# Optimization experiments

Measured on AMD Instinct MI355X. Metric: run time of the kernel, lower is better.

The kernel has to match this reference:

```python
import jax, jax.numpy as jnp
import numpy as np

HEADS = 8
SPLITS = 4


def setup_inputs() -> dict:
    key = jax.random.key(0)
    ks = jax.random.split(key, 5)
    B, C, N = 8, 512, 4096
    C2 = C // 2
    x = jax.random.normal(ks[0], (B, C, N), jnp.float32)
    # reduction: Conv1d(C -> C//2, k=1) => weight [C2, C], bias [C2]
    Wr = jax.random.normal(ks[1], (C2, C), jnp.float32) * (1.0 / np.sqrt(C))
    br = jnp.zeros((C2,), jnp.float32)
    # toQKV: Linear(C2 -> 3*C2, bias=False); stored as [in, out]
    Wqkv = jax.random.normal(ks[2], (C2, 3 * C2), jnp.float32) * (1.0 / np.sqrt(C2))
    # expansion: Conv1d(C2 -> C, k=1) => weight [C, C2], bias [C]
    We = jax.random.normal(ks[3], (C, C2), jnp.float32) * (1.0 / np.sqrt(C2))
    be = jnp.zeros((C,), jnp.float32)
    return {"x": x, "Wr": Wr, "br": br, "Wqkv": Wqkv, "We": We, "be": be}


def reference(x, Wr, br, Wqkv, We, be):
    B, C, N = x.shape
    h, S = HEADS, SPLITS
    # 1x1 conv reduction: [B, C, N] -> [B, C2, N]
    y = jnp.einsum('oc,bcn->bon', Wr, x) + br[None, :, None]
    t = y.transpose(0, 2, 1)                       # [B, N, C2]
    qkv = t @ Wqkv                                 # [B, N, 3*C2]
    q, k, v = jnp.split(qkv, 3, axis=-1)
    d = q.shape[-1] // h
    n = N // S

    def to_chunks(a):
        # b n (h d) -> b h S n' d  (block-diagonal chunks along the token dim)
        return a.reshape(B, N, h, d).transpose(0, 2, 1, 3).reshape(B, h, S, n, d)

    q, k, v = to_chunks(q), to_chunks(k), to_chunks(v)
    scale = d ** -0.5
    scores = jnp.einsum('bhsnd,bhsmd->bhsnm', q, k) * scale   # [B,h,S,n,n]
    attn = jax.nn.softmax(scores, axis=-1)
    o = jnp.einsum('bhsnm,bhsmd->bhsnd', attn, v)             # [B,h,S,n,d]
    # rearrange per-chunk to 'b n (h d)' and concat chunks along n (restores order)
    o = o.transpose(0, 2, 3, 1, 4).reshape(B, N, h * d)       # [B, N, C2]
    o = o.transpose(0, 2, 1)                                  # [B, C2, N]
    out = jnp.einsum('oc,bcn->bon', We, o) + be[None, :, None]  # [B, C, N]
    return out
```

## Files before the change

### kernel.cpp

```cpp
#include <hip/hip_runtime.h>
#include <hip/hip_bf16.h>

#define BATCH 8
#define CIN   512
#define NTOK  4096
#define CH    256
#define J3    768
#define NH    8
#define DH    32
#define NCH   1024

typedef _Float16 F16;
typedef _Float16 f16x8 __attribute__((ext_vector_type(8)));
typedef _Float16 f16x4 __attribute__((ext_vector_type(4)));
typedef _Float16 f16x2 __attribute__((ext_vector_type(2)));
typedef float    f32x4  __attribute__((ext_vector_type(4)));
typedef float    f32x16 __attribute__((ext_vector_type(16)));

#define QSCALE 0.25503483f


__global__ __launch_bounds__(256) void fuse_weights_kernel(
    const float* __restrict__ Wr, const float* __restrict__ br,
    const float* __restrict__ Wqkv,
    F16* __restrict__ Wc_t, float* __restrict__ bcomb)
{
    const int jb8 = blockIdx.x * 8;
    const int c = threadIdx.x;
    float acc0[8], acc1[8];
#pragma unroll
    for (int jj = 0; jj < 8; ++jj) { acc0[jj] = 0.f; acc1[jj] = 0.f; }
    for (int c2 = 0; c2 < CH; ++c2) {
        const float w0 = Wr[c2 * CIN + c];
        const float w1 = Wr[c2 * CIN + c + 256];
#pragma unroll
        for (int jj = 0; jj < 8; ++jj) {
            const float q = Wqkv[c2 * J3 + jb8 + jj];
            acc0[jj] = fmaf(w0, q, acc0[jj]);
            acc1[jj] = fmaf(w1, q, acc1[jj]);
        }
    }
    const int t0 = c >> 5, kg0 = (c >> 3) & 3, e0 = c & 7;
    const int c1 = c + 256;
    const int t1 = c1 >> 5, kg1 = (c1 >> 3) & 3, e1 = c1 & 7;
    const int jb = jb8 >> 8, row0 = jb8 & 255;
#pragma unroll
    for (int jj = 0; jj < 8; ++jj) {
        const float qs = (jb8 + jj < 256) ? QSCALE : 1.0f;
        const int row = row0 + jj;
        Wc_t[jb * 131072 + t0 * 8192 + kg0 * 2048 + row * 8 + e0] =
            (F16)(acc0[jj] * qs);
        Wc_t[jb * 131072 + t1 * 8192 + kg1 * 2048 + row * 8 + e1] =
            (F16)(acc1[jj] * qs);
    }
    if (c < 8) {
        const int j = jb8 + c;
        const float qs = (j < 256) ? QSCALE : 1.0f;
        float s = 0.f;
        for (int c2 = 0; c2 < CH; ++c2) s = fmaf(Wqkv[c2 * J3 + j], br[c2], s);
        bcomb[j] = s * qs;
    }
}

__global__ __launch_bounds__(256) void convert_we_kernel(
    const float* __restrict__ We, F16* __restrict__ We_t)
{
    const int i = blockIdx.x * 256 + threadIdx.x;
    const int j = i >> 8, c2 = i & 255;
    We_t[(j >> 7) * 32768 + (c2 >> 5) * 4096 + ((c2 >> 3) & 3) * 1024 +
         (j & 127) * 8 + (c2 & 7)] = (F16)We[i];
}

__global__ __launch_bounds__(256) void transpose_convert_kernel(
    const float* __restrict__ x, F16* __restrict__ xt_t)
{
    const int b = blockIdx.z;
    const int c0 = blockIdx.y * 8;
    const int n = blockIdx.x * 256 + threadIdx.x;

    const float* xb = x + ((size_t)b * CIN + c0) * NTOK + n;
    f16x8 v;
#pragma unroll
    for (int i = 0; i < 8; ++i)
        v[i] = (F16)xb[(size_t)i * NTOK];

    const int nb = n >> 7, row = n & 127;
    const int t = c0 >> 5, kg = (c0 >> 3) & 3;
    *(f16x8*)&xt_t[(size_t)b * 2097152 + nb * 65536 + t * 4096 + kg * 1024 +
                   row * 8] = v;
}

__global__ __launch_bounds__(512, 4) void gemm1_kernel(
    const F16* __restrict__ A,
    const F16* __restrict__ B,
    const float* __restrict__ bias,
    F16* __restrict__ QKb,
    F16* __restrict__ Vd)
{
    const int b  = blockIdx.z;
    const int jb = blockIdx.y;
    const int j0 = jb * 256;
    const int nb = blockIdx.x;
    const int n0 = nb * 128;
    const int tid = threadIdx.x;
    const int w = tid >> 6, l = tid & 63;
    const int wr = w >> 1;
    const int wc = w & 1;
    const int cl = l & 15, rg = l >> 4;

    __shared__ __align__(16) char smem[49152];
    F16* Ash0 = (F16*)smem;
    F16* Ash1 = (F16*)(smem + 16384);
    F16* Bsh0 = (F16*)(smem + 32768);
    F16* Bsh1 = (F16*)(smem + 40960);
    F16* Esh  = (F16*)smem;

    f32x4 acc[4][4];
#pragma unroll
    for (int i = 0; i < 4; ++i)
#pragma unroll
        for (int j = 0; j < 4; ++j) acc[i][j] = (f32x4){0.f, 0.f, 0.f, 0.f};

    const F16* Abase = A + jb * 131072 + tid * 8;
    const F16* Bbase = B + (size_t)b * 2097152 + nb * 65536 + tid * 8;

#define G1_STAGE(Adst, Bdst, t)                                                \
    do {                                                                       \
        __builtin_amdgcn_global_load_lds(                                      \
            (const __attribute__((address_space(1))) void*)(Abase + (t) * 8192),\
            (__attribute__((address_space(3))) void*)&Adst[tid * 8], 16, 0, 0);\
        __builtin_amdgcn_global_load_lds(                                      \
            (const __attribute__((address_space(1))) void*)(Abase + (t) * 8192 \
                + 4096),                                                       \
            (__attribute__((address_space(3))) void*)&Adst[4096 + tid * 8],    \
            16, 0, 0);                                                         \
        __builtin_amdgcn_global_load_lds(                                      \
            (const __attribute__((address_space(1))) void*)(Bbase + (t) * 4096),\
            (__attribute__((address_space(3))) void*)&Bdst[tid * 8], 16, 0, 0);\
    } while (0)

    G1_STAGE(Ash0, Bsh0, 0);
    __syncthreads();

    for (int t = 0; t < 16; ++t) {
        F16* Ac = (t & 1) ? Ash1 : Ash0;
        F16* Bc = (t & 1) ? Bsh1 : Bsh0;
        if (t < 15) {
            F16* An = (t & 1) ? Ash0 : Ash1;
            F16* Bn = (t & 1) ? Bsh0 : Bsh1;
            G1_STAGE(An, Bn, t + 1);
        }
        f16x8 bf[4];
#pragma unroll
        for (int j = 0; j < 4; ++j)
            bf[j] = *(const f16x8*)&Bc[rg * 1024 + (wc * 64 + j * 16 + cl) * 8];
#pragma unroll
        for (int i = 0; i < 4; ++i) {
            const f16x8 af =
                *(const f16x8*)&Ac[rg * 2048 + (wr * 64 + i * 16 + cl) * 8];
#pragma unroll
            for (int j = 0; j < 4; ++j)
                acc[i][j] = __builtin_amdgcn_mfma_f32_16x16x32_f16(
                    af, bf[j], acc[i][j], 0, 0, 0);
        }
        __syncthreads();
    }
#undef G1_STAGE

    if (j0 < 512) {
        const size_t bN = (size_t)b * NTOK;
#pragma unroll
        for (int c = 0; c < 4; ++c) {
            if (c) __syncthreads();
            if (wc == (c >> 1)) {
#pragma unroll
                for (int i = 0; i < 4; ++i) {
#pragma unroll
                    for (int jj = 0; jj < 2; ++jj) {
                        const int jn = (c & 1) * 2 + jj;
                        const int nl = jj * 16 + cl;
                        const int jl = wr * 64 + i * 16 + rg * 4;
                        const int jg = j0 + jl;
                        f16x4 v;
#pragma unroll
                        for (int r = 0; r < 4; ++r)
                            v[r] = (F16)(acc[i][jn][r] + bias[jg + r]);
                        *(f16x4*)&Esh[nl * 264 + jl] = v;
                    }
                }
            }
            __syncthreads();
            const int rr = tid >> 4, ss = tid & 15;
            const f16x8 ov0 = *(const f16x8*)&Esh[rr * 264 + ss * 16];
            const f16x8 ov1 = *(const f16x8*)&Esh[rr * 264 + ss * 16 + 8];
            F16* dst = &QKb[(bN + n0 + c * 32 + rr) * 512 + j0 + ss * 16];
            *(f16x8*)dst = ov0;
            *(f16x8*)(dst + 8) = ov1;
        }
    } else {
        const size_t bD = (size_t)b * CH;
#pragma unroll
        for (int c = 0; c < 4; ++c) {
            if (c) __syncthreads();
            if (wr == c) {
#pragma unroll
                for (int i = 0; i < 4; ++i) {
                    const int jg = j0 + c * 64 + i * 16 + rg * 4;
#pragma unroll
                    for (int jn = 0; jn < 4; ++jn) {
                        const int nl = wc * 64 + jn * 16 + cl;
#pragma unroll
                        for (int r = 0; r < 4; ++r)
                            Esh[(i * 16 + rg * 4 + r) * 136 + nl] =
                                (F16)(acc[i][jn][r] + bias[jg + r]);
                    }
                }
            }
            __syncthreads();
            const int rr = tid >> 3, ss = tid & 7;
            const f16x8 ov0 = *(const f16x8*)&Esh[rr * 136 + ss * 16];
            const f16x8 ov1 = *(const f16x8*)&Esh[rr * 136 + ss * 16 + 8];
            const int dg = (j0 - 512) + c * 64 + rr;
            F16* dst = &Vd[(bD + dg) * NTOK + n0 + ss * 16];
            *(f16x8*)dst = ov0;
            *(f16x8*)(dst + 8) = ov1;
        }
    }
}

__global__ __launch_bounds__(256) void attn_mfma_kernel(
    const F16* __restrict__ QK,
    const F16* __restrict__ Vd,
    F16* __restrict__ O)
{
    const int bid = blockIdx.x;
    const int xcd = bid & 7, tt = bid >> 3;
    const int qb = tt & 7;
    const int pr = xcd * 32 + (tt >> 3);
    const int s = pr & 3, bh = pr >> 2;
    const int b = bh >> 3, h = bh & 7;
    const int tid = threadIdx.x;
    const int w = tid >> 6, l = tid & 63;
    const int ln = l & 31;
    const int hi = l >> 5;

    __shared__ __align__(16) F16 Klds[2][64 * 40];
    __shared__ __align__(16) F16 Vlds[2][32 * 68];

    const size_t bN = (size_t)b * NTOK + (size_t)s * NCH;
    const int q0 = qb * 128 + w * 32;

    const F16* Qp = QK + (bN + q0 + ln) * 512 + h * DH + hi * 8;
    const f16x8 qf0 = *(const f16x8*)Qp;
    const f16x8 qf1 = *(const f16x8*)(Qp + 16);

    const F16* Kg = QK + (bN + (tid & 63)) * 512 + 256 + h * DH + (tid >> 6) * 8;
    const F16* Vg = Vd + ((size_t)b * CH + h * DH + (tid & 31)) * NTOK
                       + (size_t)s * NCH + (tid >> 5) * 8;
    const int kw = (tid & 63) * 40 + (tid >> 6) * 8;
    const int vw = (tid & 31) * 68 + (tid >> 5) * 8;

    f16x8 kreg = *(const f16x8*)Kg;
    f16x8 vreg = *(const f16x8*)Vg;

    const f16x8 ones = {(F16)1.f, (F16)1.f, (F16)1.f, (F16)1.f,
                        (F16)1.f, (F16)1.f, (F16)1.f, (F16)1.f};

    f32x16 oacc = (f32x16)(0.0f);
    f32x16 lacc = (f32x16)(0.0f);

    *(f16x8*)&Klds[0][kw] = kreg;
    *(f16x4*)&Vlds[0][vw] = __builtin_shufflevector(vreg, vreg, 0, 1, 2, 3);
    *(f16x4*)&Vlds[0][vw + 4] = __builtin_shufflevector(vreg, vreg, 4, 5, 6, 7);

    for (int t = 0; t < 16; ++t) {
        const int cur = t & 1, nxt = cur ^ 1;
        __syncthreads();
        if (t < 15) {
            kreg = *(const f16x8*)(Kg + (size_t)(t + 1) * 64 * 512);
            vreg = *(const f16x8*)(Vg + (t + 1) * 64);
        }
        const F16* Kb = &Klds[cur][0];
        const F16* Vb = &Vlds[cur][0];
#pragma unroll
        for (int u = 0; u < 2; ++u) {
            const int nkb = u * 32;
            const f16x8 kf0 = *(const f16x8*)&Kb[(nkb + ln) * 40 + hi * 8];
            const f16x8 kf1 = *(const f16x8*)&Kb[(nkb + ln) * 40 + 16 + hi * 8];
            f32x16 sacc = (f32x16)(0.0f);
            __builtin_amdgcn_s_setprio(1);
            sacc = __builtin_amdgcn_mfma_f32_32x32x16_f16(kf0, qf0, sacc, 0, 0, 0);
            sacc = __builtin_amdgcn_mfma_f32_32x32x16_f16(kf1, qf1, sacc, 0, 0, 0);
            __builtin_amdgcn_s_setprio(0);

            union { f16x8 v; f16x2 h[4]; } pu0, pu1;
#pragma unroll
            for (int e = 0; e < 4; ++e) {
                pu0.h[e] = __builtin_bit_cast(f16x2, __builtin_amdgcn_cvt_pkrtz(
                    __builtin_amdgcn_exp2f(sacc[2 * e]),
                    __builtin_amdgcn_exp2f(sacc[2 * e + 1])));
                pu1.h[e] = __builtin_bit_cast(f16x2, __builtin_amdgcn_cvt_pkrtz(
                    __builtin_amdgcn_exp2f(sacc[8 + 2 * e]),
                    __builtin_amdgcn_exp2f(sacc[8 + 2 * e + 1])));
            }

            const int vbase = ln * 68 + nkb + 4 * hi;
            const f16x4 v00 = *(const f16x4*)&Vb[vbase];
            const f16x4 v01 = *(const f16x4*)&Vb[vbase + 8];
            const f16x4 v10 = *(const f16x4*)&Vb[vbase + 16];
            const f16x4 v11 = *(const f16x4*)&Vb[vbase + 24];
            const f16x8 vf0 = __builtin_shufflevector(v00, v01, 0, 1, 2, 3, 4, 5, 6, 7);
            const f16x8 vf1 = __builtin_shufflevector(v10, v11, 0, 1, 2, 3, 4, 5, 6, 7);

            __builtin_amdgcn_s_setprio(1);
            oacc = __builtin_amdgcn_mfma_f32_32x32x16_f16(pu0.v, vf0, oacc, 0, 0, 0);
            oacc = __builtin_amdgcn_mfma_f32_32x32x16_f16(pu1.v, vf1, oacc, 0, 0, 0);
            lacc = __builtin_amdgcn_mfma_f32_32x32x16_f16(pu0.v, ones, lacc, 0, 0, 0);
            lacc = __builtin_amdgcn_mfma_f32_32x32x16_f16(pu1.v, ones, lacc, 0, 0, 0);
            __builtin_amdgcn_s_setprio(0);
        }
        if (t < 15) {
            *(f16x8*)&Klds[nxt][kw] = kreg;
            *(f16x4*)&Vlds[nxt][vw] =
                __builtin_shufflevector(vreg, vreg, 0, 1, 2, 3);
            *(f16x4*)&Vlds[nxt][vw + 4] =
                __builtin_shufflevector(vreg, vreg, 4, 5, 6, 7);
        }
    }

    __syncthreads();
    F16* Elds = (F16*)&Klds[0][0] + w * 1152;
#pragma unroll
    for (int r = 0; r < 16; ++r) {
        const int qr = (r & 3) + 8 * (r >> 2) + 4 * hi;
        const float invr = __builtin_amdgcn_rcpf(lacc[r]);
        Elds[qr * 36 + ln] = (F16)(oacc[r] * invr);
    }
    __syncthreads();
    F16* Ob = O + (size_t)b * 1048576 + (s * 8 + qb) * 32768 + h * 4096;
    const int q = l & 31;
#pragma unroll
    for (int st = 0; st < 2; ++st) {
        const int kg = (l >> 5) + 2 * st;
        const f16x8 ov = *(const f16x8*)&Elds[q * 36 + kg * 8];
        *(f16x8*)&Ob[kg * 1024 + (w * 32 + q) * 8] = ov;
    }
}

__global__ __launch_bounds__(256) void gemm2_kernel(
    const F16* __restrict__ A,
    const F16* __restrict__ B,
    const float* __restrict__ bias,
    float* __restrict__ Y)
{
    const int b  = blockIdx.z;
    const int jb = blockIdx.y;
    const int j0 = jb * 128;
    const int nb = blockIdx.x;
    const int n0 = nb * 128;
    const int tid = threadIdx.x;
    const int w = tid >> 6, l = tid & 63;
    const int wr = w >> 1, wc = w & 1;
    const int cl = l & 15, rg = l >> 4;

    __shared__ __align__(16) F16 Ash[2][4096];
    __shared__ __align__(16) F16 Bsh[2][4096];

    f32x4 acc[4][4];
#pragma unroll
    for (int i = 0; i < 4; ++i)
#pragma unroll
        for (int j = 0; j < 4; ++j) acc[i][j] = (f32x4){0.f, 0.f, 0.f, 0.f};

    const int frag_off = rg * 1024 + cl * 8;
    const F16* Abase = A + jb * 32768 + tid * 8;
    const F16* Bbase = B + (size_t)b * 1048576 + nb * 32768 + tid * 8;

#define G2_STAGE(bu, t)                                                        \
    do {                                                                       \
        __builtin_amdgcn_global_load_lds(                                      \
            (const __attribute__((address_space(1))) void*)(Abase + (t) * 4096),\
            (__attribute__((address_space(3))) void*)&Ash[bu][tid * 8],        \
            16, 0, 0);                                                         \
        __builtin_amdgcn_global_load_lds(                                      \
            (const __attribute__((address_space(1))) void*)(Abase + (t) * 4096 \
                + 2048),                                                       \
            (__attribute__((address_space(3))) void*)&Ash[bu][2048 + tid * 8], \
            16, 0, 0);                                                         \
        __builtin_amdgcn_global_load_lds(                                      \
            (const __attribute__((address_space(1))) void*)(Bbase + (t) * 4096),\
            (__attribute__((address_space(3))) void*)&Bsh[bu][tid * 8],        \
            16, 0, 0);                                                         \
        __builtin_amdgcn_global_load_lds(                                      \
            (const __attribute__((address_space(1))) void*)(Bbase + (t) * 4096 \
                + 2048),                                                       \
            (__attribute__((address_space(3))) void*)&Bsh[bu][2048 + tid * 8], \
            16, 0, 0);                                                         \
    } while (0)

    G2_STAGE(0, 0);
    __syncthreads();

    for (int t = 0; t < 8; ++t) {
        const int cur = t & 1;
        if (t < 7) G2_STAGE(cur ^ 1, t + 1);

        f16x8 af[4], bfr[4];
#pragma unroll
        for (int f = 0; f < 4; ++f) {
            af[f]  = *(const f16x8*)&Ash[cur][frag_off + (wr * 64 + f * 16) * 8];
            bfr[f] = *(const f16x8*)&Bsh[cur][frag_off + (wc * 64 + f * 16) * 8];
        }
#pragma unroll
        for (int i = 0; i < 4; ++i)
#pragma unroll
            for (int j = 0; j < 4; ++j)
                acc[i][j] = __builtin_amdgcn_mfma_f32_16x16x32_f16(
                    af[i], bfr[j], acc[i][j], 0, 0, 0);
        __syncthreads();
    }
#undef G2_STAGE

#pragma unroll
    for (int i = 0; i < 4; ++i) {
        const int jj = j0 + wr * 64 + i * 16 + rg * 4;
#pragma unroll
        for (int j = 0; j < 4; ++j) {
            const int nn = n0 + wc * 64 + j * 16 + cl;
#pragma unroll
            for (int r = 0; r < 4; ++r)
                Y[((size_t)b * CIN + jj + r) * NTOK + nn] =
                    acc[i][j][r] + bias[jj + r];
        }
    }
}

extern "C" void kernel_launch(void* const* d_in, const int* in_sizes, int n_in,
                              void* d_out, int out_size, void* d_ws, size_t ws_size,
                              hipStream_t stream)
{
    const float* x    = (const float*)d_in[0];
    const float* Wr   = (const float*)d_in[1];
    const float* br   = (const float*)d_in[2];
    const float* Wqkv = (const float*)d_in[3];
    const float* We   = (const float*)d_in[4];
    const float* be   = (const float*)d_in[5];
    float* out = (float*)d_out;

    char* ws = (char*)d_ws;
    F16*   Wc    = (F16*)ws;      ws += 786432;
    float* bcomb = (float*)ws;    ws += 4096;
    F16*   We_t  = (F16*)ws;      ws += 262144;
    F16*   QKb   = (F16*)ws;      ws += (size_t)BATCH * NTOK * 512 * 2;
    F16*   Vd    = (F16*)ws;      ws += (size_t)BATCH * CH * NTOK * 2;
    F16*   xt    = (F16*)ws;
    F16*   O_t   = (F16*)ws;

    fuse_weights_kernel<<<J3 / 8, 256, 0, stream>>>(Wr, br, Wqkv, Wc, bcomb);
    convert_we_kernel<<<CIN * CH / 256, 256, 0, stream>>>(We, We_t);
    transpose_convert_kernel<<<dim3(NTOK / 256, CIN / 8, BATCH), 256, 0, stream>>>(x, xt);
    gemm1_kernel<<<dim3(NTOK / 128, J3 / 256, BATCH), 512, 0, stream>>>(
        Wc, xt, bcomb, QKb, Vd);
    attn_mfma_kernel<<<2048, 256, 0, stream>>>(QKb, Vd, O_t);
    gemm2_kernel<<<dim3(NTOK / 128, CIN / 128, BATCH), 256, 0, stream>>>(
        We_t, O_t, be, out);
}
```

Measured before the change: 181.9 us.

## Write K and V in per-head tile-contiguous layout and merge row-sum MFMAs

The QKV GEMM epilogue now writes Q, K and V to separate buffers, with K and V laid out per (batch, head, split) in contiguous 64-token tiles that match the attention kernel's LDS staging pattern. Each attention tile load thus becomes one fully coalesced contiguous read instead of strided rows. The softmax row-sum also adds the two fp16 probability fragments before a single MFMA against ones, halving those MFMAs at the cost of fp16 rounding in the pre-sum.

```diff
diff --git a/kernel.cpp b/kernel.cpp
--- a/kernel.cpp
+++ b/kernel.cpp
@@ -94,8 +94,9 @@
     const F16* __restrict__ A,
     const F16* __restrict__ B,
     const float* __restrict__ bias,
-    F16* __restrict__ QKb,
-    F16* __restrict__ Vd)
+    F16* __restrict__ Qb,
+    F16* __restrict__ Kt,
+    F16* __restrict__ Vt)
 {
     const int b  = blockIdx.z;
     const int jb = blockIdx.y;
@@ -167,7 +168,10 @@
     }
 #undef G1_STAGE
 
-    if (j0 < 512) {
+    const int sidx = n0 >> 10;
+    const int tb   = (n0 >> 6) & 15;
+
+    if (jb < 2) {
         const size_t bN = (size_t)b * NTOK;
 #pragma unroll
         for (int c = 0; c < 4; ++c) {
@@ -190,15 +194,29 @@
                 }
             }
             __syncthreads();
-            const int rr = tid >> 4, ss = tid & 15;
-            const f16x8 ov0 = *(const f16x8*)&Esh[rr * 264 + ss * 16];
-            const f16x8 ov1 = *(const f16x8*)&Esh[rr * 264 + ss * 16 + 8];
-            F16* dst = &QKb[(bN + n0 + c * 32 + rr) * 512 + j0 + ss * 16];
-            *(f16x8*)dst = ov0;
-            *(f16x8*)(dst + 8) = ov1;
+            if (jb == 0) {
+                const int rr = tid >> 4, ss = tid & 15;
+                const f16x8 ov0 = *(const f16x8*)&Esh[rr * 264 + ss * 16];
+                const f16x8 ov1 = *(const f16x8*)&Esh[rr * 264 + ss * 16 + 8];
+                F16* dst = &Qb[(bN + n0 + c * 32 + rr) * 256 + ss * 16];
+                *(f16x8*)dst = ov0;
+                *(f16x8*)(dst + 8) = ov1;
+            } else {
+                const int tloc = (tb + (c >> 1)) & 15;
+#pragma unroll
+                for (int p = 0; p < 2; ++p) {
+                    const int uid = tid + p * 512;
+                    const int nl = uid & 31, kg = (uid >> 5) & 3,
+                              hh = uid >> 7;
+                    const f16x8 ov =
+                        *(const f16x8*)&Esh[nl * 264 + hh * 32 + kg * 8];
+                    const int nk = (c & 1) * 32 + nl;
+                    *(f16x8*)&Kt[(((size_t)b * NH + hh) * 4 + sidx) * 32768 +
+                                 tloc * 2048 + kg * 512 + nk * 8] = ov;
+                }
+            }
         }
     } else {
-        const size_t bD = (size_t)b * CH;
 #pragma unroll
         for (int c = 0; c < 4; ++c) {
             if (c) __syncthreads();
@@ -217,20 +235,26 @@
                 }
             }
             __syncthreads();
-            const int rr = tid >> 3, ss = tid & 7;
-            const f16x8 ov0 = *(const f16x8*)&Esh[rr * 136 + ss * 16];
-            const f16x8 ov1 = *(const f16x8*)&Esh[rr * 136 + ss * 16 + 8];
-            const int dg = (j0 - 512) + c * 64 + rr;
-            F16* dst = &Vd[(bD + dg) * NTOK + n0 + ss * 16];
-            *(f16x8*)dst = ov0;
-            *(f16x8*)(dst + 8) = ov1;
+#pragma unroll
+            for (int p = 0; p < 2; ++p) {
+                const int uid = tid + p * 512;
+                const int d = uid & 31, vg = (uid >> 5) & 7,
+                          ttv = (uid >> 8) & 1, hl = uid >> 9;
+                const int hh = c * 2 + hl;
+                const int tloc = (tb + ttv) & 15;
+                const f16x8 ov =
+                    *(const f16x8*)&Esh[(hl * 32 + d) * 136 + ttv * 64 + vg * 8];
+                *(f16x8*)&Vt[(((size_t)b * NH + hh) * 4 + sidx) * 32768 +
+                             tloc * 2048 + vg * 256 + d * 8] = ov;
+            }
         }
     }
 }
 
 __global__ __launch_bounds__(256) void attn_mfma_kernel(
-    const F16* __restrict__ QK,
-    const F16* __restrict__ Vd,
+    const F16* __restrict__ Qb,
+    const F16* __restrict__ Kt,
+    const F16* __restrict__ Vt,
     F16* __restrict__ O)
 {
     const int bid = blockIdx.x;
@@ -250,18 +274,17 @@
     const size_t bN = (size_t)b * NTOK + (size_t)s * NCH;
     const int q0 = qb * 128 + w * 32;
 
-    const F16* Qp = QK + (bN + q0 + ln) * 512 + h * DH + hi * 8;
+    const F16* Qp = Qb + (bN + q0 + ln) * 256 + h * DH + hi * 8;
     const f16x8 qf0 = *(const f16x8*)Qp;
     const f16x8 qf1 = *(const f16x8*)(Qp + 16);
 
-    const F16* Kg = QK + (bN + (tid & 63)) * 512 + 256 + h * DH + (tid >> 6) * 8;
-    const F16* Vg = Vd + ((size_t)b * CH + h * DH + (tid & 31)) * NTOK
-                       + (size_t)s * NCH + (tid >> 5) * 8;
+    const F16* Kbase = Kt + (((size_t)b * NH + h) * 4 + s) * 32768 + tid * 8;
+    const F16* Vbase = Vt + (((size_t)b * NH + h) * 4 + s) * 32768 + tid * 8;
     const int kw = (tid & 63) * 40 + (tid >> 6) * 8;
     const int vw = (tid & 31) * 68 + (tid >> 5) * 8;
 
-    f16x8 kreg = *(const f16x8*)Kg;
-    f16x8 vreg = *(const f16x8*)Vg;
+    f16x8 kreg = *(const f16x8*)Kbase;
+    f16x8 vreg = *(const f16x8*)Vbase;
 
     const f16x8 ones = {(F16)1.f, (F16)1.f, (F16)1.f, (F16)1.f,
                         (F16)1.f, (F16)1.f, (F16)1.f, (F16)1.f};
@@ -277,8 +300,8 @@
         const int cur = t & 1, nxt = cur ^ 1;
         __syncthreads();
         if (t < 15) {
-            kreg = *(const f16x8*)(Kg + (size_t)(t + 1) * 64 * 512);
-            vreg = *(const f16x8*)(Vg + (t + 1) * 64);
+            kreg = *(const f16x8*)(Kbase + (t + 1) * 2048);
+            vreg = *(const f16x8*)(Vbase + (t + 1) * 2048);
         }
         const F16* Kb = &Klds[cur][0];
         const F16* Vb = &Vlds[cur][0];
@@ -303,6 +326,7 @@
                     __builtin_amdgcn_exp2f(sacc[8 + 2 * e]),
                     __builtin_amdgcn_exp2f(sacc[8 + 2 * e + 1])));
             }
+            const f16x8 ps = pu0.v + pu1.v;
 
             const int vbase = ln * 68 + nkb + 4 * hi;
             const f16x4 v00 = *(const f16x4*)&Vb[vbase];
@@ -315,8 +339,7 @@
             __builtin_amdgcn_s_setprio(1);
             oacc = __builtin_amdgcn_mfma_f32_32x32x16_f16(pu0.v, vf0, oacc, 0, 0, 0);
             oacc = __builtin_amdgcn_mfma_f32_32x32x16_f16(pu1.v, vf1, oacc, 0, 0, 0);
-            lacc = __builtin_amdgcn_mfma_f32_32x32x16_f16(pu0.v, ones, lacc, 0, 0, 0);
-            lacc = __builtin_amdgcn_mfma_f32_32x32x16_f16(pu1.v, ones, lacc, 0, 0, 0);
+            lacc = __builtin_amdgcn_mfma_f32_32x32x16_f16(ps, ones, lacc, 0, 0, 0);
             __builtin_amdgcn_s_setprio(0);
         }
         if (t < 15) {
@@ -451,8 +474,9 @@
     F16*   Wc    = (F16*)ws;      ws += 786432;
     float* bcomb = (float*)ws;    ws += 4096;
     F16*   We_t  = (F16*)ws;      ws += 262144;
-    F16*   QKb   = (F16*)ws;      ws += (size_t)BATCH * NTOK * 512 * 2;
-    F16*   Vd    = (F16*)ws;      ws += (size_t)BATCH * CH * NTOK * 2;
+    F16*   Qb    = (F16*)ws;      ws += (size_t)BATCH * NTOK * 256 * 2;
+    F16*   Kt    = (F16*)ws;      ws += (size_t)BATCH * NH * 4 * 32768 * 2;
+    F16*   Vt    = (F16*)ws;      ws += (size_t)BATCH * NH * 4 * 32768 * 2;
     F16*   xt    = (F16*)ws;
     F16*   O_t   = (F16*)ws;
 
@@ -460,8 +484,8 @@
     convert_we_kernel<<<CIN * CH / 256, 256, 0, stream>>>(We, We_t);
     transpose_convert_kernel<<<dim3(NTOK / 256, CIN / 8, BATCH), 256, 0, stream>>>(x, xt);
     gemm1_kernel<<<dim3(NTOK / 128, J3 / 256, BATCH), 512, 0, stream>>>(
-        Wc, xt, bcomb, QKb, Vd);
-    attn_mfma_kernel<<<2048, 256, 0, stream>>>(QKb, Vd, O_t);
+        Wc, xt, bcomb, Qb, Kt, Vt);
+    attn_mfma_kernel<<<2048, 256, 0, stream>>>(Qb, Kt, Vt, O_t);
     gemm2_kernel<<<dim3(NTOK / 128, CIN / 128, BATCH), 256, 0, stream>>>(
         We_t, O_t, be, out);
 }
```

New measurement: 179.1 us. About the same (-1.5%).
